# Performance work log

Hardware: AMD Instinct MI355X
Metric: run time of the kernel (lower is better)

## Reference

```python
import jax, jax.numpy as jnp
import numpy as np

H = 64      # h_dim
E = 64      # embedding_dim
L = 100     # latent_dim
T = 30      # seq_len
DT = 0.03

def _leaky(x):
    return jnp.where(x >= 0, x, 0.01 * x)  # nn.LeakyReLU default slope

def _mlp(h, Ws, bs, Wf, bf):
    # 3 stacked [H,H] LeakyReLU layers + final [L,H] layer, LeakyReLU after EVERY layer (as in source)
    for i in range(Ws.shape[0]):
        h = _leaky(h @ Ws[i].T + bs[i])
    return _leaky(h @ Wf.T + bf)

def _lstm_step(h, c, gates):
    # torch LSTM gate order: i, f, g, o
    i, f, g, o = jnp.split(gates, 4, axis=-1)
    c = jax.nn.sigmoid(f) * c + jax.nn.sigmoid(i) * jnp.tanh(g)
    h = jax.nn.sigmoid(o) * jnp.tanh(c)
    return h, c

def _forward(expert_traj, init_state, eps,
             W_se, b_se,
             W_ih_e, W_hh_e, b_ih_e, b_hh_e,
             mean_Ws, mean_bs, mean_Wf, mean_bf,
             lv_Ws, lv_bs, lv_Wf, lv_bf,
             W_init, b_init,
             W_ih_d, W_hh_d, b_ih_d, b_hh_d,
             W_c, b_c):
    B = expert_traj.shape[0]
    # --- encode: relative positions ---
    rel_xy = jnp.concatenate([expert_traj[:, :1, :2],
                              expert_traj[:, 1:, :2] - expert_traj[:, :-1, :2]], axis=1)
    inp = jnp.concatenate([rel_xy, expert_traj[:, :, 2:]], axis=-1)  # [B,T,4]
    emb = inp @ W_se.T + b_se                                        # [B,T,E]
    x_seq = jnp.swapaxes(emb, 0, 1)                                  # [T,B,E] seq-major
    # precompute input projection for all timesteps in one GEMM
    xp = x_seq @ W_ih_e.T + (b_ih_e + b_hh_e)                        # [T,B,4H]
    h0 = jnp.zeros((B, H), dtype=expert_traj.dtype)
    c0 = jnp.zeros((B, H), dtype=expert_traj.dtype)
    def enc_step(carry, xp_t):
        h, c = carry
        h, c = _lstm_step(h, c, xp_t + h @ W_hh_e.T)
        return (h, c), None
    (hT, _), _ = jax.lax.scan(enc_step, (h0, c0), xp)
    mu = _mlp(hT, mean_Ws, mean_bs, mean_Wf, mean_bf)                # [B,L]
    log_var = _mlp(hT, lv_Ws, lv_bs, lv_Wf, lv_bf)                   # [B,L]
    # --- reparameterize + tanh ---
    z = jnp.tanh(eps * jnp.exp(0.5 * log_var) + mu)
    # --- decode ---
    dh = z @ W_init.T + b_init                                       # [B,H], h0 = c0 = dh
    bias_d = b_ih_d + b_hh_d
    def dec_step(carry, _):
        h, c, prev = carry
        xe = prev @ W_se.T + b_se                                    # spatial embedding of state
        h, c = _lstm_step(h, c, xe @ W_ih_d.T + h @ W_hh_d.T + bias_d)
        ctrl = h @ W_c.T + b_c                                       # [B,2]
        pedal = ctrl[:, 0]
        steer = jnp.clip(ctrl[:, 1], -0.5, 0.5)
        x_t, y_t, psi, v = prev[:, 0], prev[:, 1], prev[:, 2], prev[:, 3]
        v1 = jnp.clip(v + pedal * DT, 0.0, 30.0)
        psi_dot = jnp.clip(v * jnp.tan(steer) / 2.5, -3.14 / 2, 3.14 / 2)
        cur = jnp.stack([x_t + v * jnp.cos(psi) * DT,
                         y_t + v * jnp.sin(psi) * DT,
                         psi + psi_dot * DT,
                         v1], axis=1)
        return (h, c, cur), cur
    _, traj = jax.lax.scan(dec_step, (dh, dh, init_state), None, length=T)
    recons = jnp.swapaxes(traj, 0, 1)                                # [B,T,4]
    return recons, expert_traj, mu, log_var

def setup_inputs() -> dict:
    key = jax.random.key(0)
    ks = jax.random.split(key, 32)
    B = 16384
    s = 0.05
    def p(k, shape):
        return jax.random.normal(k, shape, dtype=jnp.float32) * s
    return {
        "expert_traj": jax.random.normal(ks[0], (B, T, 4), dtype=jnp.float32),
        "init_state": jax.random.normal(ks[1], (B, 4), dtype=jnp.float32),
        "eps": jax.random.normal(ks[2], (B, L), dtype=jnp.float32),
        "W_se": p(ks[3], (E, 4)), "b_se": p(ks[4], (E,)),
        "W_ih_e": p(ks[5], (4 * H, E)), "W_hh_e": p(ks[6], (4 * H, H)),
        "b_ih_e": p(ks[7], (4 * H,)), "b_hh_e": p(ks[8], (4 * H,)),
        "mean_Ws": p(ks[9], (3, H, H)), "mean_bs": p(ks[10], (3, H)),
        "mean_Wf": p(ks[11], (L, H)), "mean_bf": p(ks[12], (L,)),
        "lv_Ws": p(ks[13], (3, H, H)), "lv_bs": p(ks[14], (3, H)),
        "lv_Wf": p(ks[15], (L, H)), "lv_bf": p(ks[16], (L,)),
        "W_init": p(ks[17], (H, L)), "b_init": p(ks[18], (H,)),
        "W_ih_d": p(ks[19], (4 * H, E)), "W_hh_d": p(ks[20], (4 * H, H)),
        "b_ih_d": p(ks[21], (4 * H,)), "b_hh_d": p(ks[22], (4 * H,)),
        "W_c": p(ks[23], (2, H)), "b_c": p(ks[24], (2,)),
    }

def reference(expert_traj, init_state, eps,
              W_se, b_se,
              W_ih_e, W_hh_e, b_ih_e, b_hh_e,
              mean_Ws, mean_bs, mean_Wf, mean_bf,
              lv_Ws, lv_bs, lv_Wf, lv_bf,
              W_init, b_init,
              W_ih_d, W_hh_d, b_ih_d, b_hh_d,
              W_c, b_c):
    return _forward(expert_traj, init_state, eps,
                    W_se, b_se,
                    W_ih_e, W_hh_e, b_ih_e, b_hh_e,
                    mean_Ws, mean_bs, mean_Wf, mean_bf,
                    lv_Ws, lv_bs, lv_Wf, lv_bf,
                    W_init, b_init,
                    W_ih_d, W_hh_d, b_ih_d, b_hh_d,
                    W_c, b_c)
```

## Files before the change

### kernel.cpp

```cpp
#include <hip/hip_runtime.h>

typedef unsigned short u16;
typedef unsigned int u32;
typedef __attribute__((ext_vector_type(8))) short bf16x8;
typedef __attribute__((ext_vector_type(4))) float f32x4;

#define B_TOT 16384
#define RR 32
#define BLK 512
#define NBLK (B_TOT / RR)
#define TT 30
#define LL 100
#define DTC 0.03f
#define L2E 1.44269504088896f

#define HST 104
#define HBUF_U16 (RR * HST)

#define OFF_H   0
#define OFF_XB  13312
#define OFF_Z   22528
#define OFF_U   31232
#define SMEM_SZ 38912

#define WS_WHHE  0
#define WS_WHHD  18432
#define WS_MWS   36864
#define WS_LWS   49152
#define WS_MWF   61440
#define WS_LWF   67840
#define WS_WINIT 74240
#define WS_TOTAL 82432

__device__ __forceinline__ float bf2f(u16 u) {
    union { u32 i; float f; } v; v.i = ((u32)u) << 16; return v.f;
}
__device__ __forceinline__ u16 f2bf(float f) {
    union { float f; u32 i; } v; v.f = f;
    return (u16)((v.i + 0x7FFFu + ((v.i >> 16) & 1u)) >> 16);
}
__device__ __forceinline__ u16 f2bf_t(float f) {
    union { float f; u32 i; } v; v.f = f;
    return (u16)(v.i >> 16);
}
__device__ __forceinline__ float rcpf(float x) { return __builtin_amdgcn_rcpf(x); }
__device__ __forceinline__ float ex2(float x) { return __builtin_amdgcn_exp2f(x); }
__device__ __forceinline__ float tanh_(float x) {
    x = fminf(fmaxf(x, -15.f), 15.f);
    float e = __expf(2.f * x);
    return (e - 1.f) * rcpf(e + 1.f);
}
__device__ __forceinline__ float leaky(float x) { return x >= 0.f ? x : 0.01f * x; }
__device__ __forceinline__ f32x4 mfma16(bf16x8 a, bf16x8 b, f32x4 c) {
    return __builtin_amdgcn_mfma_f32_16x16x32_bf16(a, b, c, 0, 0, 0);
}

__global__ void setup_kernel(
    const float* __restrict__ W_se, const float* __restrict__ b_se,
    const float* __restrict__ W_ih_e, const float* __restrict__ W_hh_e,
    const float* __restrict__ b_ih_e, const float* __restrict__ b_hh_e,
    const float* __restrict__ W_ih_d, const float* __restrict__ W_hh_d,
    const float* __restrict__ b_ih_d, const float* __restrict__ b_hh_d,
    const float* __restrict__ mean_Ws, const float* __restrict__ lv_Ws,
    const float* __restrict__ mean_Wf, const float* __restrict__ lv_Wf,
    const float* __restrict__ W_init, u16* __restrict__ ws)
{
    const int gid = blockIdx.x * 256 + threadIdx.x;
    const int nth = gridDim.x * 256;
    for (int i = gid; i < 512; i += nth) {
        int which = i >> 8, row = i & 255, g = row >> 6;
        float s = (g == 2) ? 2.f * L2E : L2E;
        const float* wih = (which ? W_ih_d : W_ih_e) + row * 64;
        float f0=0,f1=0,f2=0,f3=0,fb=0;
        for (int e = 0; e < 64; ++e) {
            float w = wih[e];
            f0 = fmaf(w, W_se[e*4+0], f0);
            f1 = fmaf(w, W_se[e*4+1], f1);
            f2 = fmaf(w, W_se[e*4+2], f2);
            f3 = fmaf(w, W_se[e*4+3], f3);
            fb = fmaf(w, b_se[e], fb);
        }
        fb += (which ? b_ih_d : b_ih_e)[row] + (which ? b_hh_d : b_hh_e)[row];
        u16* dst = ws + (which ? WS_WHHD : WS_WHHE) + row * 72 + 64;
        dst[0]=f2bf(f0*s); dst[1]=f2bf(f1*s); dst[2]=f2bf(f2*s); dst[3]=f2bf(f3*s);
        dst[4]=f2bf(fb*s); dst[5]=0; dst[6]=0; dst[7]=0;
    }
    for (int i = gid; i < 2*16384; i += nth) {
        int which = i >= 16384;
        int j = which ? i - 16384 : i;
        int row = j >> 6, k = j & 63, g = row >> 6;
        float s = (g == 2) ? 2.f * L2E : L2E;
        const float* whh = which ? W_hh_d : W_hh_e;
        ws[(which ? WS_WHHD : WS_WHHE) + row*72 + k] = f2bf(whh[j] * s);
    }
    for (int i = gid; i < 12288; i += nth) {
        ws[WS_MWS + i] = f2bf(mean_Ws[i]);
        ws[WS_LWS + i] = f2bf(lv_Ws[i]);
    }
    for (int i = gid; i < 6400; i += nth) {
        ws[WS_MWF + i] = f2bf(mean_Wf[i]);
        ws[WS_LWF + i] = f2bf(lv_Wf[i]);
    }
    for (int i = gid; i < 8192; i += nth) {
        int r = i >> 7, k = i & 127;
        ws[WS_WINIT + i] = (k < LL) ? f2bf(W_init[r*LL + k]) : (u16)0;
    }
}

__global__ __launch_bounds__(BLK, 4) void vae_lstm_kernel(
    const float* __restrict__ expert, const float* __restrict__ init_state,
    const float* __restrict__ eps, const u16* __restrict__ ws,
    const float* __restrict__ mean_bs, const float* __restrict__ mean_bf,
    const float* __restrict__ lv_bs, const float* __restrict__ lv_bf,
    const float* __restrict__ b_init, const float* __restrict__ W_c,
    const float* __restrict__ b_c,
    float* __restrict__ out_recons, float* __restrict__ out_expert,
    float* __restrict__ out_mu, float* __restrict__ out_lv)
{
    const int tid = threadIdx.x;
    const int b0g = blockIdx.x * RR;
    const int wv = tid >> 6;
    const int Mt = wv >> 2;
    const int wsub = wv & 3;
    const int lane = tid & 63;
    const int lcol = lane & 15;
    const int quad = lane >> 4;
    const int jcol = wsub * 16 + lcol;

    __shared__ __align__(16) char smem[SMEM_SZ];
    u16* Hbuf  = (u16*)(smem + OFF_H);
    u16* XB0   = (u16*)(smem + OFF_XB);
    u16* XB1   = XB0 + RR * 72;
    u16* zBuf  = (u16*)(smem + OFF_Z);
    u16* inp   = (u16*)(smem + OFF_U);
    u16* muB   = (u16*)(smem + OFF_U);
    float* sRaw  = (float*)(smem + OFF_XB);
    float* sc    = (float*)(smem + OFF_XB);

    {
        const int base = b0g * (TT*4);
        u32* hz = (u32*)Hbuf;
        for (int idx = tid; idx < HBUF_U16; idx += BLK) hz[idx] = 0;
        for (int idx = tid; idx < RR*TT*4; idx += BLK) {
            float v = expert[base + idx];
            sRaw[idx] = v;
            out_expert[base + idx] = v;
        }
        __syncthreads();
        for (int idx = tid; idx < RR*TT*4; idx += BLK) {
            int q = idx % (TT*4);
            int k = q & 3, t = q >> 2;
            int row = idx / (TT*4);
            float v = sRaw[idx];
            if (k < 2 && t > 0) v -= sRaw[idx - 4];
            u16 hv = f2bf(v);
            inp[idx] = hv;
            if (t == 0) Hbuf[row*HST + 64 + k] = hv;
            if (q == 0) {
                Hbuf[row*HST + 68] = 0x3F80;
                Hbuf[HBUF_U16 + row*HST + 68] = 0x3F80;
            }
        }
        __syncthreads();
    }

    float creg[4] = {0.f, 0.f, 0.f, 0.f};
    float hval[4];
    bf16x8 bw[4][3];

    auto build_bw = [&](const u16* wsW) {
#pragma unroll
        for (int g = 0; g < 4; ++g) {
            const u16* wr = wsW + (g*64 + jcol) * 72;
            bw[g][0] = *(const bf16x8*)(wr + quad*8);
            bw[g][1] = *(const bf16x8*)(wr + 32 + quad*8);
            bw[g][2] = *(const bf16x8*)(wr + 64);
        }
    };

    auto lstm_step = [&](const u16* Hc, u16* Hn) {
        const u16* hrow = Hc + (Mt*16 + lcol)*HST;
        bf16x8 a0 = *(const bf16x8*)(hrow + quad*8);
        bf16x8 a1 = *(const bf16x8*)(hrow + 32 + quad*8);
        bf16x8 a2 = *(const bf16x8*)(hrow + 64 + quad*8);
        f32x4 acc[4];
#pragma unroll
        for (int g = 0; g < 4; ++g) {
            f32x4 z = {0.f, 0.f, 0.f, 0.f};
            z = mfma16(a0, bw[g][0], z);
            z = mfma16(a1, bw[g][1], z);
            acc[g] = mfma16(a2, bw[g][2], z);
        }
#pragma unroll
        for (int r = 0; r < 4; ++r) {
            float Ei = ex2(-acc[0][r]);
            float Ef = ex2(-acc[1][r]);
            float Eg = ex2(-acc[2][r]);
            float Eo = ex2(-acc[3][r]);
            float P = (1.f + Ei) * (1.f + Eg);
            float Q = 1.f + Ef;
            float num = fmaf(creg[r], P, (1.f - Eg) * Q);
            float cc = num * rcpf(P * Q);
            creg[r] = cc;
            float Ec = ex2(-2.f * L2E * cc);
            float h = (1.f - Ec) * rcpf((1.f + Eo) * (1.f + Ec));
            hval[r] = h;
            Hn[(Mt*16 + quad*4 + r)*HST + jcol] = f2bf_t(h);
        }
    };

    build_bw(ws + WS_WHHE);
    for (int stp = 0; stp < TT; ++stp) {
        const u16* Hc = Hbuf + (stp & 1) * HBUF_U16;
        u16* Hn = Hbuf + ((stp + 1) & 1) * HBUF_U16;
        lstm_step(Hc, Hn);
        if (tid < 128 && stp < TT-1) {
            int row = tid >> 2, k = tid & 3;
            Hn[row*HST + 64 + k] = inp[row*(TT*4) + (stp+1)*4 + k];
        }
        __syncthreads();
    }

    {
        u32* zb = (u32*)zBuf;
        for (int idx = tid; idx < RR*136/2; idx += BLK) zb[idx] = 0;
    }

    auto mlp_hidden = [&](const u16* inB, int inStride, u16* outB,
                          const u16* wsW, const float* bg) {
        float bv = bg[jcol];
        const u16* wr = wsW + jcol*64;
        bf16x8 bb0 = *(const bf16x8*)(wr + quad*8);
        bf16x8 bb1 = *(const bf16x8*)(wr + 32 + quad*8);
        f32x4 acc = {bv, bv, bv, bv};
        bf16x8 a0 = *(const bf16x8*)(inB + (Mt*16 + lcol)*inStride + quad*8);
        bf16x8 a1 = *(const bf16x8*)(inB + (Mt*16 + lcol)*inStride + 32 + quad*8);
        acc = mfma16(a0, bb0, acc);
        acc = mfma16(a1, bb1, acc);
#pragma unroll
        for (int r = 0; r < 4; ++r)
            outB[(Mt*16 + quad*4 + r)*72 + jcol] = f2bf_t(leaky(acc[r]));
        __syncthreads();
    };

    auto mlp_final = [&](const u16* inB, const u16* wsW, const float* bg, int mode) {
#pragma unroll
        for (int ti = 0; ti < 2; ++ti) {
            int t = wv + ti*8;
            if (t >= 14) continue;
            int nt = t >> 1, Mtl = t & 1;
            int n = nt*16 + lcol;
            bool ok = (n < LL);
            float bv = ok ? bg[n] : 0.f;
            bf16x8 bb0, bb1;
            if (ok) {
                const u16* wr = wsW + n*64;
                bb0 = *(const bf16x8*)(wr + quad*8);
                bb1 = *(const bf16x8*)(wr + 32 + quad*8);
            } else {
#pragma unroll
                for (int j = 0; j < 8; ++j) { bb0[j] = 0; bb1[j] = 0; }
            }
            f32x4 acc = {bv, bv, bv, bv};
            bf16x8 a0 = *(const bf16x8*)(inB + (Mtl*16 + lcol)*72 + quad*8);
            bf16x8 a1 = *(const bf16x8*)(inB + (Mtl*16 + lcol)*72 + 32 + quad*8);
            acc = mfma16(a0, bb0, acc);
            acc = mfma16(a1, bb1, acc);
            if (ok) {
#pragma unroll
                for (int r = 0; r < 4; ++r) {
                    int m = Mtl*16 + quad*4 + r;
                    float vv = leaky(acc[r]);
                    size_t gi = (size_t)(b0g + m) * LL + n;
                    if (mode == 0) {
                        muB[m*LL + n] = f2bf_t(vv);
                        out_mu[gi] = vv;
                    } else {
                        out_lv[gi] = vv;
                        float mu = bf2f(muB[m*LL + n]);
                        float zv = tanh_(fmaf(eps[gi], __expf(0.5f * vv), mu));
                        zBuf[m*136 + n] = f2bf_t(zv);
                    }
                }
            }
        }
        __syncthreads();
    };

    mlp_hidden(Hbuf, HST, XB0, ws + WS_MWS, mean_bs);
    mlp_hidden(XB0, 72, XB1, ws + WS_MWS + 4096, mean_bs + 64);
    mlp_hidden(XB1, 72, XB0, ws + WS_MWS + 8192, mean_bs + 128);
    mlp_final(XB0, ws + WS_MWF, mean_bf, 0);
    mlp_hidden(Hbuf, HST, XB0, ws + WS_LWS, lv_bs);
    mlp_hidden(XB0, 72, XB1, ws + WS_LWS + 4096, lv_bs + 64);
    mlp_hidden(XB1, 72, XB0, ws + WS_LWS + 8192, lv_bs + 128);
    mlp_final(XB0, ws + WS_LWF, lv_bf, 1);

    {
        float bv = b_init[jcol];
        const u16* wr = ws + WS_WINIT + jcol*128;
        f32x4 acc = {bv, bv, bv, bv};
#pragma unroll
        for (int kt = 0; kt < 4; ++kt) {
            bf16x8 az = *(const bf16x8*)(zBuf + (Mt*16 + lcol)*136 + kt*32 + quad*8);
            bf16x8 bi = *(const bf16x8*)(wr + kt*32 + quad*8);
            acc = mfma16(az, bi, acc);
        }
#pragma unroll
        for (int r = 0; r < 4; ++r) {
            creg[r] = acc[r];
            Hbuf[(Mt*16 + quad*4 + r)*HST + jcol] = f2bf_t(acc[r]);
        }
        __syncthreads();
        if (tid < RR*4) {
            int row = tid >> 2, k = tid & 3;
            Hbuf[row*HST + 64 + k] = f2bf(init_state[b0g*4 + tid]);
        }
        __syncthreads();
    }

    float px = 0.f, py = 0.f, ppsi = 0.f, pv = 0.f;
    if (tid < 32) {
        const float* is = init_state + (size_t)(b0g + tid)*4;
        px = is[0]; py = is[1]; ppsi = is[2]; pv = is[3];
    }
    const float wc0 = W_c[jcol];
    const float wc1 = W_c[64 + jcol];
    const float bc0 = b_c[0], bc1 = b_c[1];
    build_bw(ws + WS_WHHD);

    for (int stp = 0; stp < TT; ++stp) {
        const u16* Hc = Hbuf + (stp & 1) * HBUF_U16;
        u16* Hn = Hbuf + ((stp + 1) & 1) * HBUF_U16;
        lstm_step(Hc, Hn);
        float pa[4], pb[4];
#pragma unroll
        for (int r = 0; r < 4; ++r) {
            pa[r] = hval[r] * wc0;
            pb[r] = hval[r] * wc1;
        }
#pragma unroll
        for (int d = 1; d < 16; d <<= 1) {
#pragma unroll
            for (int r = 0; r < 4; ++r) {
                pa[r] += __shfl_xor(pa[r], d);
                pb[r] += __shfl_xor(pb[r], d);
            }
        }
        if (lcol == 0) {
#pragma unroll
            for (int r = 0; r < 4; ++r) {
                sc[Mt*128 + wsub*32 + quad*4 + r]      = pa[r];
                sc[Mt*128 + wsub*32 + 16 + quad*4 + r] = pb[r];
            }
        }
        __syncthreads();
        if (tid < 32) {
            int row = tid, Mt2 = tid >> 4, ri = tid & 15;
            const float* s = sc + Mt2*128;
            float pedal = s[ri] + s[32 + ri] + s[64 + ri] + s[96 + ri] + bc0;
            float s1 = s[16 + ri] + s[48 + ri] + s[80 + ri] + s[112 + ri] + bc1;
            float steer = fminf(fmaxf(s1, -0.5f), 0.5f);
            float v1 = fminf(fmaxf(pv + pedal * DTC, 0.f), 30.f);
            float sn, cs;
            __sincosf(ppsi, &sn, &cs);
            float psid = fminf(fmaxf(pv * __tanf(steer) * 0.4f, -1.57f), 1.57f);
            float nx = fmaf(pv * cs, DTC, px);
            float ny = fmaf(pv * sn, DTC, py);
            float npsi = fmaf(psid, DTC, ppsi);
            px = nx; py = ny; ppsi = npsi; pv = v1;
            float4 o; o.x = nx; o.y = ny; o.z = npsi; o.w = v1;
            *(float4*)(out_recons + ((size_t)(b0g + row) * TT + stp) * 4) = o;
            u32 lo = (u32)f2bf(nx) | ((u32)f2bf(ny) << 16);
            u32 hi = (u32)f2bf(npsi) | ((u32)f2bf(v1) << 16);
            uint2 pk; pk.x = lo; pk.y = hi;
            *(uint2*)(Hn + row*HST + 64) = pk;
        }
        __syncthreads();
    }
}

extern "C" void kernel_launch(void* const* d_in, const int* in_sizes, int n_in,
                              void* d_out, int out_size, void* d_ws, size_t ws_size,
                              hipStream_t stream) {
    (void)in_sizes; (void)n_in; (void)ws_size; (void)out_size;
    const float* expert    = (const float*)d_in[0];
    const float* init_st   = (const float*)d_in[1];
    const float* eps       = (const float*)d_in[2];
    const float* W_se      = (const float*)d_in[3];
    const float* b_se      = (const float*)d_in[4];
    const float* W_ih_e    = (const float*)d_in[5];
    const float* W_hh_e    = (const float*)d_in[6];
    const float* b_ih_e    = (const float*)d_in[7];
    const float* b_hh_e    = (const float*)d_in[8];
    const float* mean_Ws   = (const float*)d_in[9];
    const float* mean_bs   = (const float*)d_in[10];
    const float* mean_Wf   = (const float*)d_in[11];
    const float* mean_bf   = (const float*)d_in[12];
    const float* lv_Ws     = (const float*)d_in[13];
    const float* lv_bs     = (const float*)d_in[14];
    const float* lv_Wf     = (const float*)d_in[15];
    const float* lv_bf     = (const float*)d_in[16];
    const float* W_init    = (const float*)d_in[17];
    const float* b_init    = (const float*)d_in[18];
    const float* W_ih_d    = (const float*)d_in[19];
    const float* W_hh_d    = (const float*)d_in[20];
    const float* b_ih_d    = (const float*)d_in[21];
    const float* b_hh_d    = (const float*)d_in[22];
    const float* W_c       = (const float*)d_in[23];
    const float* b_c       = (const float*)d_in[24];

    float* out = (float*)d_out;
    const size_t n_traj = (size_t)B_TOT * TT * 4;
    const size_t n_lat  = (size_t)B_TOT * LL;
    float* out_recons = out;
    float* out_expert = out + n_traj;
    float* out_mu     = out + 2 * n_traj;
    float* out_lv     = out + 2 * n_traj + n_lat;

    u16* ws = (u16*)d_ws;

    setup_kernel<<<64, 256, 0, stream>>>(
        W_se, b_se, W_ih_e, W_hh_e, b_ih_e, b_hh_e,
        W_ih_d, W_hh_d, b_ih_d, b_hh_d,
        mean_Ws, lv_Ws, mean_Wf, lv_Wf, W_init, ws);

    vae_lstm_kernel<<<NBLK, BLK, 0, stream>>>(
        expert, init_st, eps, ws,
        mean_bs, mean_bf, lv_bs, lv_bf, b_init, W_c, b_c,
        out_recons, out_expert, out_mu, out_lv);
}
```

Measured before the change: 235.2 us.

## Compute decoder control head from bf16 hidden state with 128 threads

```diff
diff --git a/kernel.cpp b/kernel.cpp
--- a/kernel.cpp
+++ b/kernel.cpp
@@ -135,7 +135,8 @@
     u16* inp   = (u16*)(smem + OFF_U);
     u16* muB   = (u16*)(smem + OFF_U);
     float* sRaw  = (float*)(smem + OFF_XB);
-    float* sc    = (float*)(smem + OFF_XB);
+    float* sPrev = (float*)(smem + OFF_XB);
+    float* sWc   = (float*)(smem + OFF_XB + 512);
 
     {
         const int base = b0g * (TT*4);
@@ -165,7 +166,6 @@
     }
 
     float creg[4] = {0.f, 0.f, 0.f, 0.f};
-    float hval[4];
     bf16x8 bw[4][3];
 
     auto build_bw = [&](const u16* wsW) {
@@ -174,7 +174,14 @@
             const u16* wr = wsW + (g*64 + jcol) * 72;
             bw[g][0] = *(const bf16x8*)(wr + quad*8);
             bw[g][1] = *(const bf16x8*)(wr + 32 + quad*8);
-            bw[g][2] = *(const bf16x8*)(wr + 64);
+            if (quad == 0) {
+                bw[g][2] = *(const bf16x8*)(wr + 64);
+            } else {
+                bf16x8 z;
+#pragma unroll
+                for (int j = 0; j < 8; ++j) z[j] = 0;
+                bw[g][2] = z;
+            }
         }
     };
 
@@ -204,7 +211,6 @@
             creg[r] = cc;
             float Ec = ex2(-2.f * L2E * cc);
             float h = (1.f - Ec) * rcpf((1.f + Eo) * (1.f + Ec));
-            hval[r] = h;
             Hn[(Mt*16 + quad*4 + r)*HST + jcol] = f2bf_t(h);
         }
     };
@@ -313,68 +319,69 @@
         }
         __syncthreads();
         if (tid < RR*4) {
-            int row = tid >> 2, k = tid & 3;
-            Hbuf[row*HST + 64 + k] = f2bf(init_state[b0g*4 + tid]);
-        }
-        __syncthreads();
-    }
-
-    float px = 0.f, py = 0.f, ppsi = 0.f, pv = 0.f;
-    if (tid < 32) {
-        const float* is = init_state + (size_t)(b0g + tid)*4;
-        px = is[0]; py = is[1]; ppsi = is[2]; pv = is[3];
-    }
-    const float wc0 = W_c[jcol];
-    const float wc1 = W_c[64 + jcol];
+            float v = init_state[b0g*4 + tid];
+            sPrev[tid] = v;
+            Hbuf[(tid >> 2)*HST + 64 + (tid & 3)] = f2bf(v);
+        }
+        if (tid < 128) sWc[tid] = W_c[tid];
+        __syncthreads();
+    }
+
+    build_bw(ws + WS_WHHD);
     const float bc0 = b_c[0], bc1 = b_c[1];
-    build_bw(ws + WS_WHHD);
 
     for (int stp = 0; stp < TT; ++stp) {
         const u16* Hc = Hbuf + (stp & 1) * HBUF_U16;
         u16* Hn = Hbuf + ((stp + 1) & 1) * HBUF_U16;
         lstm_step(Hc, Hn);
-        float pa[4], pb[4];
-#pragma unroll
-        for (int r = 0; r < 4; ++r) {
-            pa[r] = hval[r] * wc0;
-            pb[r] = hval[r] * wc1;
-        }
-#pragma unroll
-        for (int d = 1; d < 16; d <<= 1) {
-#pragma unroll
-            for (int r = 0; r < 4; ++r) {
-                pa[r] += __shfl_xor(pa[r], d);
-                pb[r] += __shfl_xor(pb[r], d);
-            }
-        }
-        if (lcol == 0) {
-#pragma unroll
-            for (int r = 0; r < 4; ++r) {
-                sc[Mt*128 + wsub*32 + quad*4 + r]      = pa[r];
-                sc[Mt*128 + wsub*32 + 16 + quad*4 + r] = pb[r];
-            }
-        }
-        __syncthreads();
-        if (tid < 32) {
-            int row = tid, Mt2 = tid >> 4, ri = tid & 15;
-            const float* s = sc + Mt2*128;
-            float pedal = s[ri] + s[32 + ri] + s[64 + ri] + s[96 + ri] + bc0;
-            float s1 = s[16 + ri] + s[48 + ri] + s[80 + ri] + s[112 + ri] + bc1;
-            float steer = fminf(fmaxf(s1, -0.5f), 0.5f);
-            float v1 = fminf(fmaxf(pv + pedal * DTC, 0.f), 30.f);
-            float sn, cs;
-            __sincosf(ppsi, &sn, &cs);
-            float psid = fminf(fmaxf(pv * __tanf(steer) * 0.4f, -1.57f), 1.57f);
-            float nx = fmaf(pv * cs, DTC, px);
-            float ny = fmaf(pv * sn, DTC, py);
-            float npsi = fmaf(psid, DTC, ppsi);
-            px = nx; py = ny; ppsi = npsi; pv = v1;
-            float4 o; o.x = nx; o.y = ny; o.z = npsi; o.w = v1;
-            *(float4*)(out_recons + ((size_t)(b0g + row) * TT + stp) * 4) = o;
-            u32 lo = (u32)f2bf(nx) | ((u32)f2bf(ny) << 16);
-            u32 hi = (u32)f2bf(npsi) | ((u32)f2bf(v1) << 16);
-            uint2 pk; pk.x = lo; pk.y = hi;
-            *(uint2*)(Hn + row*HST + 64) = pk;
+        __syncthreads();
+        if (tid < 128) {
+            int row = tid >> 2, kq = tid & 3;
+            const u16* hr = Hn + row*HST + kq*16;
+            bf16x8 h0 = *(const bf16x8*)(hr);
+            bf16x8 h1 = *(const bf16x8*)(hr + 8);
+            const float4* w0 = (const float4*)(sWc + kq*16);
+            const float4* w1 = (const float4*)(sWc + 64 + kq*16);
+            float a0 = 0.f, a1 = 0.f;
+#pragma unroll
+            for (int p = 0; p < 2; ++p) {
+                float4 wa = w0[2*p], wb = w0[2*p+1];
+                float4 va = w1[2*p], vb = w1[2*p+1];
+                bf16x8 hh = p ? h1 : h0;
+                float hf[8];
+#pragma unroll
+                for (int j = 0; j < 8; ++j) hf[j] = bf2f((u16)hh[j]);
+                a0 = fmaf(hf[0], wa.x, a0); a0 = fmaf(hf[1], wa.y, a0);
+                a0 = fmaf(hf[2], wa.z, a0); a0 = fmaf(hf[3], wa.w, a0);
+                a0 = fmaf(hf[4], wb.x, a0); a0 = fmaf(hf[5], wb.y, a0);
+                a0 = fmaf(hf[6], wb.z, a0); a0 = fmaf(hf[7], wb.w, a0);
+                a1 = fmaf(hf[0], va.x, a1); a1 = fmaf(hf[1], va.y, a1);
+                a1 = fmaf(hf[2], va.z, a1); a1 = fmaf(hf[3], va.w, a1);
+                a1 = fmaf(hf[4], vb.x, a1); a1 = fmaf(hf[5], vb.y, a1);
+                a1 = fmaf(hf[6], vb.z, a1); a1 = fmaf(hf[7], vb.w, a1);
+            }
+            a0 += __shfl_xor(a0, 1); a1 += __shfl_xor(a1, 1);
+            a0 += __shfl_xor(a0, 2); a1 += __shfl_xor(a1, 2);
+            if (kq == 0) {
+                float pedal = a0 + bc0;
+                float steer = fminf(fmaxf(a1 + bc1, -0.5f), 0.5f);
+                float4 pv = *(const float4*)(sPrev + row*4);
+                float x = pv.x, y = pv.y, psi = pv.z, v = pv.w;
+                float v1 = fminf(fmaxf(v + pedal * DTC, 0.f), 30.f);
+                float sn, cs;
+                __sincosf(psi, &sn, &cs);
+                float psid = fminf(fmaxf(v * __tanf(steer) * 0.4f, -1.57f), 1.57f);
+                float nx = fmaf(v * cs, DTC, x);
+                float ny = fmaf(v * sn, DTC, y);
+                float npsi = fmaf(psid, DTC, psi);
+                float4 o; o.x = nx; o.y = ny; o.z = npsi; o.w = v1;
+                *(float4*)(sPrev + row*4) = o;
+                *(float4*)(out_recons + ((size_t)(b0g + row) * TT + stp) * 4) = o;
+                u32 lo = (u32)f2bf(nx) | ((u32)f2bf(ny) << 16);
+                u32 hi = (u32)f2bf(npsi) | ((u32)f2bf(v1) << 16);
+                uint2 pk; pk.x = lo; pk.y = hi;
+                *(uint2*)(Hn + row*HST + 64) = pk;
+            }
         }
         __syncthreads();
     }
```

New measurement: 209.2 us. 11.1% less time.
